# Kernel tuning notes

Measured on AMD Instinct MI355X. Metric: run time of the kernel, lower is better.

The kernel has to match this reference:

```python
import jax, jax.numpy as jnp
import numpy as np

ATTN_MASK_VALUE = -1e10
HEADS, DIM_HEAD, WSZ = 8, 64, 512


def ln(x, scale, eps=1e-5):
    # haiku LayerNorm(create_scale=True, create_offset=False, axis=-1)
    m = x.mean(-1, keepdims=True)
    v = ((x - m) ** 2).mean(-1, keepdims=True)
    return (x - m) / jnp.sqrt(v + eps) * scale


def local_attn(x, ln_s, qkv_w, ow, ob):
    n, _ = x.shape
    w = n // WSZ
    xn = ln(x, ln_s)
    qkv = xn @ qkv_w                                   # [n, 3*h*d]
    q, k, v = jnp.split(qkv, 3, axis=-1)
    resh = lambda t: t.reshape(w, WSZ, HEADS, DIM_HEAD).transpose(2, 0, 1, 3)  # h w n d
    q, k, v = resh(q), resh(k), resh(v)
    def lookback(t):
        t = jnp.pad(t, ((0, 0), (1, 0), (0, 0), (0, 0)))
        return jnp.concatenate((t[:, :-1], t[:, 1:]), axis=2)  # h w 2*wsz d
    k, v = lookback(k), lookback(v)
    sim = jnp.einsum('hwid,hwjd->hwij', q, k) * (DIM_HEAD ** -0.5)
    mask = jnp.tril(jnp.ones((WSZ, 2 * WSZ), dtype=bool), WSZ)
    sim = jnp.where(mask, sim, ATTN_MASK_VALUE)
    attn = jax.nn.softmax(sim, axis=-1)
    out = jnp.einsum('hwij,hwjd->hwid', attn, v)
    out = out.transpose(1, 2, 0, 3).reshape(n, HEADS * DIM_HEAD)
    return out @ ow + ob


def feedforward(x, ln_s, w1, b1, w2, b2):
    xn = ln(x, ln_s)
    return jax.nn.gelu(xn @ w1 + b1) @ w2 + b2


def gmlp(x, ln_s, win, bin_, sln, sw, sb, sow, sob, pow_, pob):
    n = x.shape[0]
    xn = ln(x, ln_s)
    h = jax.nn.gelu(xn @ win + bin_)                   # [n, d_ff]
    xg, gate = jnp.split(h, 2, axis=-1)                # [n, d_ff/2] each
    gate = ln(gate, sln)
    wm = sw * jnp.tril(jnp.ones((n, n), dtype=sw.dtype))
    gate = jnp.einsum('nd,mn->md', gate, wm) + sb      # causal spatial gate
    s = (xg * gate) @ sow + sob
    return s @ pow_ + pob


def forward(tokens, embed, attn_ln, attn_qkv, attn_ow, attn_ob,
            ff_ln, ff_w1, ff_b1, ff_w2, ff_b2,
            g_ln, g_win, g_bin, g_sln, g_sw, g_sb, g_sow, g_sob, g_pow, g_pob,
            fin_ln, head_w, head_b):
    x = embed[tokens]                                  # [n, dim]

    def block(xc, p):
        xc = xc + local_attn(xc, p['al'], p['aq'], p['aw'], p['ab'])
        xc = xc + feedforward(xc, p['fl'], p['f1'], p['fb1'], p['f2'], p['fb2'])
        return xc, None

    attn_params = {'al': attn_ln, 'aq': attn_qkv, 'aw': attn_ow, 'ab': attn_ob,
                   'fl': ff_ln, 'f1': ff_w1, 'fb1': ff_b1, 'f2': ff_w2, 'fb2': ff_b2}
    x, _ = jax.lax.scan(block, x, attn_params)

    def gblock(xc, p):
        xc = xc + gmlp(xc, p['l'], p['wi'], p['bi'], p['sl'], p['sw'], p['sb'],
                       p['so'], p['sob'], p['po'], p['pob'])
        return xc, None

    g_params = {'l': g_ln, 'wi': g_win, 'bi': g_bin, 'sl': g_sln, 'sw': g_sw,
                'sb': g_sb, 'so': g_sow, 'sob': g_sob, 'po': g_pow, 'pob': g_pob}
    x, _ = jax.lax.scan(gblock, x, g_params)

    return ln(x, fin_ln) @ head_w + head_b             # [n, num_tokens]


def setup_inputs() -> dict:
    key = jax.random.key(0)
    ks = jax.random.split(key, 16)
    n, dim, dff, inner, depth, gdepth, vocab = 2048, 1024, 4096, 512, 6, 2, 32
    sc = 0.02
    eps_sgu = 0.001 / n
    return {
        'tokens': jax.random.randint(ks[0], (n,), 0, vocab),
        'embed': jax.random.normal(ks[1], (vocab, dim)) * sc,
        'attn_ln': jnp.ones((depth, dim)),
        'attn_qkv': jax.random.normal(ks[2], (depth, dim, 3 * inner)) * sc,
        'attn_ow': jax.random.normal(ks[3], (depth, inner, dim)) * sc,
        'attn_ob': jnp.zeros((depth, dim)),
        'ff_ln': jnp.ones((depth, dim)),
        'ff_w1': jax.random.normal(ks[4], (depth, dim, dff)) * sc,
        'ff_b1': jnp.zeros((depth, dff)),
        'ff_w2': jax.random.normal(ks[5], (depth, dff, dim)) * sc,
        'ff_b2': jnp.zeros((depth, dim)),
        'g_ln': jnp.ones((gdepth, dim)),
        'g_win': jax.random.normal(ks[6], (gdepth, dim, dff)) * sc,
        'g_bin': jnp.zeros((gdepth, dff)),
        'g_sln': jnp.ones((gdepth, dff // 2)),
        'g_sw': jax.random.uniform(ks[7], (gdepth, n, n), minval=-eps_sgu, maxval=eps_sgu),
        'g_sb': jnp.ones((gdepth, n, 1)),
        'g_sow': jax.random.normal(ks[8], (gdepth, dff // 2, dff // 2)) * sc,
        'g_sob': jnp.zeros((gdepth, dff // 2)),
        'g_pow': jax.random.normal(ks[9], (gdepth, dff // 2, dim)) * sc,
        'g_pob': jnp.zeros((gdepth, dim)),
        'fin_ln': jnp.ones((dim,)),
        'head_w': jax.random.normal(ks[10], (dim, vocab)) * sc,
        'head_b': jnp.zeros((vocab,)),
    }


def reference(tokens, embed, attn_ln, attn_qkv, attn_ow, attn_ob,
              ff_ln, ff_w1, ff_b1, ff_w2, ff_b2,
              g_ln, g_win, g_bin, g_sln, g_sw, g_sb, g_sow, g_sob, g_pow, g_pob,
              fin_ln, head_w, head_b):
    return forward(tokens, embed, attn_ln, attn_qkv, attn_ow, attn_ob,
                   ff_ln, ff_w1, ff_b1, ff_w2, ff_b2,
                   g_ln, g_win, g_bin, g_sln, g_sw, g_sb, g_sow, g_sob, g_pow, g_pob,
                   fin_ln, head_w, head_b)
```

## Files before the change

### kernel.cpp

```cpp
#include <hip/hip_runtime.h>
#include <hip/hip_bf16.h>
#include <math.h>

using bf16 = __hip_bfloat16;
typedef __bf16 bf16x8 __attribute__((ext_vector_type(8)));
typedef float f32x4 __attribute__((ext_vector_type(4)));

__device__ __forceinline__ float toF(float v) { return v; }
__device__ __forceinline__ float toF(bf16 v) { return __bfloat162float(v); }

__device__ __forceinline__ float gelu_f(float x) {
  float t = tanhf(0.7978845608028654f * (x + 0.044715f * x * x * x));
  return 0.5f * x * (1.0f + t);
}

__device__ __forceinline__ void gld_lds16(const bf16* g, bf16* l) {
  __builtin_amdgcn_global_load_lds(
      (const __attribute__((address_space(1))) void*)g,
      (__attribute__((address_space(3))) void*)l, 16, 0, 0);
}

__device__ __forceinline__ float block_sum(float v) {
  __shared__ float tmp[8];
  int lane = threadIdx.x & 63, w = threadIdx.x >> 6, nw = blockDim.x >> 6;
#pragma unroll
  for (int o = 32; o > 0; o >>= 1) v += __shfl_down(v, o, 64);
  __syncthreads();
  if (lane == 0) tmp[w] = v;
  __syncthreads();
  float r = 0.f;
  for (int i = 0; i < nw; ++i) r += tmp[i];
  return r;
}

__device__ __forceinline__ float block_max(float v) {
  __shared__ float tmp2[8];
  int lane = threadIdx.x & 63, w = threadIdx.x >> 6, nw = blockDim.x >> 6;
#pragma unroll
  for (int o = 32; o > 0; o >>= 1) v = fmaxf(v, __shfl_down(v, o, 64));
  __syncthreads();
  if (lane == 0) tmp2[w] = v;
  __syncthreads();
  float r = -1e30f;
  for (int i = 0; i < nw; ++i) r = fmaxf(r, tmp2[i]);
  return r;
}

template <int BM, int BN, int EPI>
__launch_bounds__((BM / 64) * (BN / 64) * 64)
__global__ void gemm_bt(const bf16* __restrict__ A, int lda, long sAzh, long sAzw,
                        const bf16* __restrict__ B, int ldb, long sBzh, long sBzw,
                        void* __restrict__ C, int ldc, long sCzh, long sCzw,
                        int M, int N, int K, int zdiv,
                        const float* __restrict__ bias,
                        const float* __restrict__ rowbias,
                        const bf16* __restrict__ mul, int ldmul,
                        float* __restrict__ resid, int trilskip,
                        int nxk, int kchunk) {
  constexpr int BK = 32;
  constexpr int WM = BM / 64, WN = BN / 64;
  constexpr int NT = WM * WN * 64;
  __shared__ __align__(16) bf16 As[BM * BK];
  __shared__ __align__(16) bf16 Bs[BN * BK];
  const int tid = threadIdx.x;
  const int wave = tid >> 6, lane = tid & 63;
  const int wm = wave / WN, wn = wave % WN;
  int bx = blockIdx.x, kc = 0;
  if (kchunk > 0) { kc = bx / nxk; bx -= kc * nxk; }
  const int m0 = blockIdx.y * BM, n0 = bx * BN;
  const int z = blockIdx.z;
  const int zh = z / zdiv, zw = z % zdiv;
  A += zh * sAzh + zw * sAzw;
  B += zh * sBzh + zw * sBzw;
  const long coff = zh * sCzh + zw * sCzw;

  f32x4 acc[4][4];
#pragma unroll
  for (int i = 0; i < 4; ++i)
#pragma unroll
    for (int j = 0; j < 4; ++j)
#pragma unroll
      for (int r = 0; r < 4; ++r) acc[i][j][r] = 0.0f;

  const int kbeg = (kchunk > 0) ? kc * kchunk : 0;
  int kend = K;
  if (kchunk > 0 && kbeg + kchunk < kend) kend = kbeg + kchunk;
  if (trilskip && m0 + BM < kend) kend = m0 + BM;
  const int lrow = lane & 15, lk = (lane >> 4) << 3;

  for (int k0 = kbeg; k0 < kend; k0 += BK) {
#pragma unroll
    for (int c = 0; c < (BM * BK) / (NT * 8); ++c) {
      int e = (c * NT + tid) << 3;
      int r = e >> 5, kk = e & 31;
      gld_lds16(A + (long)(m0 + r) * lda + (k0 + kk), As + e);
    }
#pragma unroll
    for (int c = 0; c < (BN * BK) / (NT * 8); ++c) {
      int e = (c * NT + tid) << 3;
      int r = e >> 5, kk = e & 31;
      gld_lds16(B + (long)(n0 + r) * ldb + (k0 + kk), Bs + e);
    }
    __syncthreads();
    if (trilskip && (k0 + BK > m0)) {
#pragma unroll
      for (int c = 0; c < (BM * BK) / (NT * 8); ++c) {
        int e = (c * NT + tid) << 3;
        int r = e >> 5, kk = e & 31;
        int m = m0 + r;
#pragma unroll
        for (int q = 0; q < 8; ++q)
          if (k0 + kk + q > m) As[e + q] = __float2bfloat16(0.0f);
      }
      __syncthreads();
    }
    bf16x8 af[4], bg[4];
#pragma unroll
    for (int i = 0; i < 4; ++i)
      af[i] = *(const bf16x8*)(As + (wm * 64 + i * 16 + lrow) * BK + lk);
#pragma unroll
    for (int j = 0; j < 4; ++j)
      bg[j] = *(const bf16x8*)(Bs + (wn * 64 + j * 16 + lrow) * BK + lk);
#pragma unroll
    for (int i = 0; i < 4; ++i)
#pragma unroll
      for (int j = 0; j < 4; ++j)
        acc[i][j] = __builtin_amdgcn_mfma_f32_16x16x32_bf16(af[i], bg[j], acc[i][j], 0, 0, 0);
    __syncthreads();
  }

  const int rbase = m0 + wm * 64 + ((lane >> 4) << 2);
  const int cbase = n0 + wn * 64 + (lane & 15);
#pragma unroll
  for (int i = 0; i < 4; ++i) {
#pragma unroll
    for (int j = 0; j < 4; ++j) {
#pragma unroll
      for (int r = 0; r < 4; ++r) {
        int row = rbase + i * 16 + r;
        int col = cbase + j * 16;
        float v = acc[i][j][r];
        long idx = coff + (long)row * ldc + col;
        if (EPI == 0) {
          if (bias) v += bias[col];
          ((bf16*)C)[idx] = __float2bfloat16(v);
        } else if (EPI == 2) {
          v += bias[col];
          ((bf16*)C)[idx] = __float2bfloat16(gelu_f(v));
        } else if (EPI == 3) {
          if (kchunk > 0) {
            if (kbeg == 0) v += bias[col];
            atomicAdd(&resid[idx], v);
          } else {
            v += bias[col];
            resid[idx] += v;
          }
        } else if (EPI == 4) {
          v += rowbias[row];
          v *= __bfloat162float(mul[(long)row * ldmul + col]);
          ((bf16*)C)[idx] = __float2bfloat16(v);
        }
      }
    }
  }
}

__global__ void k_embed(const int* __restrict__ tokens, const float* __restrict__ embed,
                        float* __restrict__ x) {
  int t = blockIdx.x;
  int tok = tokens[t];
  for (int j = threadIdx.x; j < 1024; j += 256)
    x[(long)t * 1024 + j] = embed[(long)tok * 1024 + j];
}

template <typename TIN>
__global__ void k_ln(const TIN* __restrict__ in, int ldin, const float* __restrict__ scale,
                     bf16* __restrict__ out, int ldout, int C) {
  int row = blockIdx.x, tid = threadIdx.x;
  const TIN* p = in + (long)row * ldin;
  float loc[8];
  int nper = C >> 8;
  float s = 0.f;
  for (int c = 0; c < nper; ++c) {
    float v = toF(p[c * 256 + tid]);
    loc[c] = v;
    s += v;
  }
  s = block_sum(s);
  float mean = s / (float)C;
  float s2 = 0.f;
  for (int c = 0; c < nper; ++c) {
    float d = loc[c] - mean;
    s2 += d * d;
  }
  s2 = block_sum(s2);
  float inv = 1.0f / sqrtf(s2 / (float)C + 1e-5f);
  for (int c = 0; c < nper; ++c) {
    int j = c * 256 + tid;
    out[(long)row * ldout + j] = __float2bfloat16((loc[c] - mean) * inv * scale[j]);
  }
}

template <typename TIN>
__global__ void k_transpose(const TIN* __restrict__ in, int ldin, bf16* __restrict__ out,
                            int ldout, int rows, int cols) {
  __shared__ bf16 tile[32][33];
  int c0 = blockIdx.x * 32, r0 = blockIdx.y * 32;
  int tx = threadIdx.x & 31, ty = threadIdx.x >> 5;
#pragma unroll
  for (int j = 0; j < 32; j += 8)
    tile[ty + j][tx] = __float2bfloat16(toF(in[(long)(r0 + ty + j) * ldin + c0 + tx]));
  __syncthreads();
#pragma unroll
  for (int j = 0; j < 32; j += 8)
    out[(long)(c0 + ty + j) * ldout + r0 + tx] = tile[tx][ty + j];
}

__global__ void k_cast(const float* __restrict__ in, bf16* __restrict__ out, long n) {
  long i = (long)blockIdx.x * 256 + threadIdx.x;
  if (i < n) out[i] = __float2bfloat16(in[i]);
}

__global__ void k_packk(const bf16* __restrict__ qkv, bf16* __restrict__ kpad) {
  int idx = blockIdx.x * 256 + threadIdx.x;
  int d = idx & 63, t = (idx >> 6) & 2047, h = idx >> 17;
  kpad[(long)h * 163840 + (512 + t) * 64 + d] = qkv[(long)t * 1536 + 512 + h * 64 + d];
}

__global__ void k_zeropad(bf16* __restrict__ kpad, bf16* __restrict__ vtpad) {
  int idx = blockIdx.x * 256 + threadIdx.x;
  bf16 z = __float2bfloat16(0.0f);
  if (idx < 262144) {
    int h = idx >> 15, off = idx & 32767;
    kpad[(long)h * 163840 + off] = z;
  } else {
    int i = idx - 262144;
    int f = i >> 9, j = i & 511;
    vtpad[(long)f * 2560 + j] = z;
  }
}

__global__ void k_softmax(bf16* __restrict__ SP) {
  int row = blockIdx.x;
  int i = row & 511;
  int limit = i + 513;
  bf16* s = SP + (long)row * 1024;
  int tid = threadIdx.x;
  float v[4];
  float mx = -1e30f;
#pragma unroll
  for (int c = 0; c < 4; ++c) {
    int j = c * 256 + tid;
    float xv = (j < limit) ? __bfloat162float(s[j]) * 0.125f : -1e30f;
    v[c] = xv;
    mx = fmaxf(mx, xv);
  }
  mx = block_max(mx);
  float sum = 0.f;
#pragma unroll
  for (int c = 0; c < 4; ++c) {
    float e = (v[c] <= -1e29f) ? 0.f : expf(v[c] - mx);
    v[c] = e;
    sum += e;
  }
  sum = block_sum(sum);
  float inv = 1.0f / sum;
#pragma unroll
  for (int c = 0; c < 4; ++c) {
    int j = c * 256 + tid;
    s[j] = __float2bfloat16(v[c] * inv);
  }
}

__global__ void k_head(const float* __restrict__ x, const float* __restrict__ sc,
                       const float* __restrict__ w, const float* __restrict__ b,
                       float* __restrict__ out) {
  int row = blockIdx.x, tid = threadIdx.x;
  __shared__ float xn[1024];
  const float* p = x + (long)row * 1024;
  float loc[4];
  float s = 0.f;
#pragma unroll
  for (int c = 0; c < 4; ++c) {
    float v = p[c * 256 + tid];
    loc[c] = v;
    s += v;
  }
  s = block_sum(s);
  float mean = s / 1024.f;
  float s2 = 0.f;
#pragma unroll
  for (int c = 0; c < 4; ++c) {
    float d = loc[c] - mean;
    s2 += d * d;
  }
  s2 = block_sum(s2);
  float inv = 1.0f / sqrtf(s2 / 1024.f + 1e-5f);
#pragma unroll
  for (int c = 0; c < 4; ++c) {
    int j = c * 256 + tid;
    xn[j] = (loc[c] - mean) * inv * sc[j];
  }
  __syncthreads();
  int t = tid & 31, sl = tid >> 5;
  float partial = 0.f;
  for (int kk = 0; kk < 128; ++kk) {
    int k = sl * 128 + kk;
    partial += xn[k] * w[k * 32 + t];
  }
  __shared__ float red[256];
  red[tid] = partial;
  __syncthreads();
  if (tid < 32) {
    float r = 0.f;
    for (int q = 0; q < 8; ++q) r += red[q * 32 + t];
    out[(long)row * 32 + t] = r + b[t];
  }
}

extern "C" void kernel_launch(void* const* d_in, const int* in_sizes, int n_in,
                              void* d_out, int out_size, void* d_ws, size_t ws_size,
                              hipStream_t stream) {
  (void)in_sizes; (void)n_in; (void)out_size; (void)ws_size;
  const int*   tokens   = (const int*)d_in[0];
  const float* embed    = (const float*)d_in[1];
  const float* attn_ln  = (const float*)d_in[2];
  const float* attn_qkv = (const float*)d_in[3];
  const float* attn_ow  = (const float*)d_in[4];
  const float* attn_ob  = (const float*)d_in[5];
  const float* ff_ln    = (const float*)d_in[6];
  const float* ff_w1    = (const float*)d_in[7];
  const float* ff_b1    = (const float*)d_in[8];
  const float* ff_w2    = (const float*)d_in[9];
  const float* ff_b2    = (const float*)d_in[10];
  const float* g_ln     = (const float*)d_in[11];
  const float* g_win    = (const float*)d_in[12];
  const float* g_bin    = (const float*)d_in[13];
  const float* g_sln    = (const float*)d_in[14];
  const float* g_sw     = (const float*)d_in[15];
  const float* g_sb     = (const float*)d_in[16];
  const float* g_sow    = (const float*)d_in[17];
  const float* g_sob    = (const float*)d_in[18];
  const float* g_pow    = (const float*)d_in[19];
  const float* g_pob    = (const float*)d_in[20];
  const float* fin_ln   = (const float*)d_in[21];
  const float* head_w   = (const float*)d_in[22];
  const float* head_b   = (const float*)d_in[23];

  char* ws = (char*)d_ws;
  float* x  = (float*)ws;
  bf16* xn  = (bf16*)(ws + 8388608);
  char* SC  = ws + 12582912;
  bf16* qkv   = (bf16*)SC;
  bf16* kpad  = (bf16*)(SC + 6291456);
  bf16* vtpad = (bf16*)(SC + 8912896);
  bf16* SP    = (bf16*)(SC + 11534336);
  bf16* att   = (bf16*)(SC + 45088768);
  bf16* h      = (bf16*)SC;
  bf16* gateLN = (bf16*)(SC + 16777216);
  bf16* gateT  = (bf16*)(SC + 25165824);
  bf16* prod   = (bf16*)(SC + 33554432);
  bf16* sbuf   = (bf16*)(SC + 41943040);
  bf16* W  = (bf16*)(ws + 62914560);
  bf16* W2 = (bf16*)(ws + 71303168);

  k_embed<<<2048, 256, 0, stream>>>(tokens, embed, x);

  for (int L = 0; L < 6; ++L) {
    const float* qkvw = attn_qkv + (long)L * 1024 * 1536;
    const float* oww  = attn_ow + (long)L * 512 * 1024;
    const float* w1   = ff_w1 + (long)L * 1024 * 4096;
    const float* w2   = ff_w2 + (long)L * 4096 * 1024;

    k_ln<float><<<2048, 256, 0, stream>>>(x, 1024, attn_ln + L * 1024, xn, 1024, 1024);
    k_transpose<float><<<dim3(48, 32), 256, 0, stream>>>(qkvw, 1536, W, 1024, 1024, 1536);
    gemm_bt<128, 128, 0><<<dim3(12, 16, 1), 256, 0, stream>>>(
        xn, 1024, 0, 0, W, 1024, 0, 0, qkv, 1536, 0, 0,
        2048, 1536, 1024, 1, nullptr, nullptr, nullptr, 0, nullptr, 0, 0, 0);

    k_packk<<<4096, 256, 0, stream>>>(qkv, kpad);
    k_zeropad<<<2048, 256, 0, stream>>>(kpad, vtpad);
    k_transpose<bf16><<<dim3(16, 64), 256, 0, stream>>>(qkv + 1024, 1536, vtpad + 512, 2560, 2048, 512);

    gemm_bt<128, 128, 0><<<dim3(8, 4, 32), 256, 0, stream>>>(
        qkv, 1536, 64, 786432, kpad, 64, 163840, 32768, SP, 1024, 2097152, 524288,
        512, 1024, 64, 4, nullptr, nullptr, nullptr, 0, nullptr, 0, 0, 0);
    k_softmax<<<16384, 256, 0, stream>>>(SP);
    gemm_bt<128, 64, 0><<<dim3(1, 4, 32), 128, 0, stream>>>(
        SP, 1024, 2097152, 524288, vtpad, 2560, 163840, 512, att, 512, 64, 262144,
        512, 64, 1024, 4, nullptr, nullptr, nullptr, 0, nullptr, 0, 0, 0);
    k_transpose<float><<<dim3(32, 16), 256, 0, stream>>>(oww, 1024, W, 512, 512, 1024);
    gemm_bt<128, 128, 3><<<dim3(16, 16, 1), 256, 0, stream>>>(
        att, 512, 0, 0, W, 512, 0, 0, nullptr, 1024, 0, 0,
        2048, 1024, 512, 1, attn_ob + L * 1024, nullptr, nullptr, 0, x, 0, 8, 256);

    k_ln<float><<<2048, 256, 0, stream>>>(x, 1024, ff_ln + L * 1024, xn, 1024, 1024);
    k_transpose<float><<<dim3(128, 32), 256, 0, stream>>>(w1, 4096, W, 1024, 1024, 4096);
    gemm_bt<128, 128, 2><<<dim3(32, 16, 1), 256, 0, stream>>>(
        xn, 1024, 0, 0, W, 1024, 0, 0, h, 4096, 0, 0,
        2048, 4096, 1024, 1, ff_b1 + L * 4096, nullptr, nullptr, 0, nullptr, 0, 0, 0);
    k_transpose<float><<<dim3(32, 128), 256, 0, stream>>>(w2, 1024, W, 4096, 4096, 1024);
    gemm_bt<128, 128, 3><<<dim3(32, 16, 1), 256, 0, stream>>>(
        h, 4096, 0, 0, W, 4096, 0, 0, nullptr, 1024, 0, 0,
        2048, 1024, 4096, 1, ff_b2 + L * 1024, nullptr, nullptr, 0, x, 0, 8, 1024);
  }

  for (int G = 0; G < 2; ++G) {
    const float* winw = g_win + (long)G * 1024 * 4096;
    const float* soww = g_sow + (long)G * 2048 * 2048;
    const float* poww = g_pow + (long)G * 2048 * 1024;

    k_ln<float><<<2048, 256, 0, stream>>>(x, 1024, g_ln + G * 1024, xn, 1024, 1024);
    k_transpose<float><<<dim3(128, 32), 256, 0, stream>>>(winw, 4096, W, 1024, 1024, 4096);
    gemm_bt<128, 128, 2><<<dim3(32, 16, 1), 256, 0, stream>>>(
        xn, 1024, 0, 0, W, 1024, 0, 0, h, 4096, 0, 0,
        2048, 4096, 1024, 1, g_bin + G * 4096, nullptr, nullptr, 0, nullptr, 0, 0, 0);
    k_ln<bf16><<<2048, 256, 0, stream>>>(h + 2048, 4096, g_sln + G * 2048, gateLN, 2048, 2048);
    k_transpose<bf16><<<dim3(64, 64), 256, 0, stream>>>(gateLN, 2048, gateT, 2048, 2048, 2048);
    k_cast<<<16384, 256, 0, stream>>>(g_sw + (long)G * 2048 * 2048, W2, 4194304L);
    gemm_bt<128, 128, 4><<<dim3(16, 16, 1), 256, 0, stream>>>(
        W2, 2048, 0, 0, gateT, 2048, 0, 0, prod, 2048, 0, 0,
        2048, 2048, 2048, 1, nullptr, g_sb + G * 2048, h, 4096, nullptr, 1, 0, 0);
    k_transpose<float><<<dim3(64, 64), 256, 0, stream>>>(soww, 2048, W, 2048, 2048, 2048);
    gemm_bt<128, 128, 0><<<dim3(16, 16, 1), 256, 0, stream>>>(
        prod, 2048, 0, 0, W, 2048, 0, 0, sbuf, 2048, 0, 0,
        2048, 2048, 2048, 1, g_sob + G * 2048, nullptr, nullptr, 0, nullptr, 0, 0, 0);
    k_transpose<float><<<dim3(32, 64), 256, 0, stream>>>(poww, 1024, W, 2048, 2048, 1024);
    gemm_bt<128, 128, 3><<<dim3(32, 16, 1), 256, 0, stream>>>(
        sbuf, 2048, 0, 0, W, 2048, 0, 0, nullptr, 1024, 0, 0,
        2048, 1024, 2048, 1, g_pob + G * 1024, nullptr, nullptr, 0, x, 0, 8, 512);
  }

  k_head<<<2048, 256, 0, stream>>>(x, fin_ln, head_w, head_b, (float*)d_out);
}
```

Before: 2.350 ms.

## Double-buffer GEMM LDS tiles with BK=64 and split-K the attention PV product

The GEMM kernel gains template parameters for K-tile depth (now 64) and double-buffering, so the next tile's global-to-LDS load is issued while the current tile is computed. Most GEMMs switch to the double-buffered BK=64 variant. The attn·V GEMM, which previously launched only 128 blocks, is split four ways along K with fp32 atomic accumulation into a zeroed buffer and a cast back to bf16. This raises parallelism at the cost of extra zero/cast kernels and atomics. The double-buffered path has no barrier between issuing async global_load_lds and reading the buffer, so it may race.

```diff
diff --git a/kernel.cpp b/kernel.cpp
--- a/kernel.cpp
+++ b/kernel.cpp
@@ -46,7 +46,7 @@
   return r;
 }
 
-template <int BM, int BN, int EPI>
+template <int BM, int BN, int EPI, int BK, int DBUF>
 __launch_bounds__((BM / 64) * (BN / 64) * 64)
 __global__ void gemm_bt(const bf16* __restrict__ A, int lda, long sAzh, long sAzw,
                         const bf16* __restrict__ B, int ldb, long sBzh, long sBzw,
@@ -57,11 +57,13 @@
                         const bf16* __restrict__ mul, int ldmul,
                         float* __restrict__ resid, int trilskip,
                         int nxk, int kchunk) {
-  constexpr int BK = 32;
+  constexpr int LBK = (BK == 64) ? 6 : 5;
   constexpr int WM = BM / 64, WN = BN / 64;
   constexpr int NT = WM * WN * 64;
-  __shared__ __align__(16) bf16 As[BM * BK];
-  __shared__ __align__(16) bf16 Bs[BN * BK];
+  constexpr int ACH = (BM * BK) / (NT * 8);
+  constexpr int BCH = (BN * BK) / (NT * 8);
+  __shared__ __align__(16) bf16 As[(DBUF ? 2 : 1) * BM * BK];
+  __shared__ __align__(16) bf16 Bs[(DBUF ? 2 : 1) * BN * BK];
   const int tid = threadIdx.x;
   const int wave = tid >> 6, lane = tid & 63;
   const int wm = wave / WN, wn = wave % WN;
@@ -88,45 +90,73 @@
   if (trilskip && m0 + BM < kend) kend = m0 + BM;
   const int lrow = lane & 15, lk = (lane >> 4) << 3;
 
-  for (int k0 = kbeg; k0 < kend; k0 += BK) {
-#pragma unroll
-    for (int c = 0; c < (BM * BK) / (NT * 8); ++c) {
+  auto stage = [&](int sel, int k0) {
+    bf16* Ad = As + sel * BM * BK;
+    bf16* Bd = Bs + sel * BN * BK;
+#pragma unroll
+    for (int c = 0; c < ACH; ++c) {
       int e = (c * NT + tid) << 3;
-      int r = e >> 5, kk = e & 31;
-      gld_lds16(A + (long)(m0 + r) * lda + (k0 + kk), As + e);
-    }
-#pragma unroll
-    for (int c = 0; c < (BN * BK) / (NT * 8); ++c) {
+      int r = e >> LBK, kk = e & (BK - 1);
+      gld_lds16(A + (long)(m0 + r) * lda + (k0 + kk), Ad + e);
+    }
+#pragma unroll
+    for (int c = 0; c < BCH; ++c) {
       int e = (c * NT + tid) << 3;
-      int r = e >> 5, kk = e & 31;
-      gld_lds16(B + (long)(n0 + r) * ldb + (k0 + kk), Bs + e);
-    }
+      int r = e >> LBK, kk = e & (BK - 1);
+      gld_lds16(B + (long)(n0 + r) * ldb + (k0 + kk), Bd + e);
+    }
+  };
+  auto zero_diag = [&](int sel, int k0) {
+    bf16* Ad = As + sel * BM * BK;
+#pragma unroll
+    for (int c = 0; c < ACH; ++c) {
+      int e = (c * NT + tid) << 3;
+      int r = e >> LBK, kk = e & (BK - 1);
+      int m = m0 + r;
+#pragma unroll
+      for (int q = 0; q < 8; ++q)
+        if (k0 + kk + q > m) Ad[e + q] = __float2bfloat16(0.0f);
+    }
+  };
+  auto compute = [&](int sel) {
+    const bf16* Ad = As + sel * BM * BK;
+    const bf16* Bd = Bs + sel * BN * BK;
+#pragma unroll
+    for (int kk2 = 0; kk2 < BK; kk2 += 32) {
+      bf16x8 af[4], bg[4];
+#pragma unroll
+      for (int i = 0; i < 4; ++i)
+        af[i] = *(const bf16x8*)(Ad + (wm * 64 + i * 16 + lrow) * BK + kk2 + lk);
+#pragma unroll
+      for (int j = 0; j < 4; ++j)
+        bg[j] = *(const bf16x8*)(Bd + (wn * 64 + j * 16 + lrow) * BK + kk2 + lk);
+#pragma unroll
+      for (int i = 0; i < 4; ++i)
+#pragma unroll
+        for (int j = 0; j < 4; ++j)
+          acc[i][j] = __builtin_amdgcn_mfma_f32_16x16x32_bf16(af[i], bg[j], acc[i][j], 0, 0, 0);
+    }
+  };
+
+  if constexpr (DBUF) {
+    int cur = 0;
+    stage(0, kbeg);
     __syncthreads();
-    if (trilskip && (k0 + BK > m0)) {
-#pragma unroll
-      for (int c = 0; c < (BM * BK) / (NT * 8); ++c) {
-        int e = (c * NT + tid) << 3;
-        int r = e >> 5, kk = e & 31;
-        int m = m0 + r;
-#pragma unroll
-        for (int q = 0; q < 8; ++q)
-          if (k0 + kk + q > m) As[e + q] = __float2bfloat16(0.0f);
-      }
+    for (int k0 = kbeg; k0 < kend; k0 += BK) {
+      if (k0 + BK < kend) stage(cur ^ 1, k0 + BK);
+      if (trilskip && (k0 + BK > m0)) { zero_diag(cur, k0); __syncthreads(); }
+      compute(cur);
       __syncthreads();
-    }
-    bf16x8 af[4], bg[4];
-#pragma unroll
-    for (int i = 0; i < 4; ++i)
-      af[i] = *(const bf16x8*)(As + (wm * 64 + i * 16 + lrow) * BK + lk);
-#pragma unroll
-    for (int j = 0; j < 4; ++j)
-      bg[j] = *(const bf16x8*)(Bs + (wn * 64 + j * 16 + lrow) * BK + lk);
-#pragma unroll
-    for (int i = 0; i < 4; ++i)
-#pragma unroll
-      for (int j = 0; j < 4; ++j)
-        acc[i][j] = __builtin_amdgcn_mfma_f32_16x16x32_bf16(af[i], bg[j], acc[i][j], 0, 0, 0);
-    __syncthreads();
+      cur ^= 1;
+    }
+  } else {
+    for (int k0 = kbeg; k0 < kend; k0 += BK) {
+      stage(0, k0);
+      __syncthreads();
+      if (trilskip && (k0 + BK > m0)) { zero_diag(0, k0); __syncthreads(); }
+      compute(0);
+      __syncthreads();
+    }
   }
 
   const int rbase = m0 + wm * 64 + ((lane >> 4) << 2);
@@ -149,10 +179,10 @@
           ((bf16*)C)[idx] = __float2bfloat16(gelu_f(v));
         } else if (EPI == 3) {
           if (kchunk > 0) {
-            if (kbeg == 0) v += bias[col];
+            if (kbeg == 0 && bias) v += bias[col];
             atomicAdd(&resid[idx], v);
           } else {
-            v += bias[col];
+            if (bias) v += bias[col];
             resid[idx] += v;
           }
         } else if (EPI == 4) {
@@ -219,6 +249,11 @@
 __global__ void k_cast(const float* __restrict__ in, bf16* __restrict__ out, long n) {
   long i = (long)blockIdx.x * 256 + threadIdx.x;
   if (i < n) out[i] = __float2bfloat16(in[i]);
+}
+
+__global__ void k_zerof(float* __restrict__ p, long n) {
+  long i = (long)blockIdx.x * 256 + threadIdx.x;
+  if (i < n) p[i] = 0.0f;
 }
 
 __global__ void k_packk(const bf16* __restrict__ qkv, bf16* __restrict__ kpad) {
@@ -363,6 +398,7 @@
   bf16* sbuf   = (bf16*)(SC + 41943040);
   bf16* W  = (bf16*)(ws + 62914560);
   bf16* W2 = (bf16*)(ws + 71303168);
+  float* att_f32 = (float*)(ws + 71303168);
 
   k_embed<<<2048, 256, 0, stream>>>(tokens, embed, x);
 
@@ -374,7 +410,7 @@
 
     k_ln<float><<<2048, 256, 0, stream>>>(x, 1024, attn_ln + L * 1024, xn, 1024, 1024);
     k_transpose<float><<<dim3(48, 32), 256, 0, stream>>>(qkvw, 1536, W, 1024, 1024, 1536);
-    gemm_bt<128, 128, 0><<<dim3(12, 16, 1), 256, 0, stream>>>(
+    gemm_bt<128, 128, 0, 64, 1><<<dim3(12, 16, 1), 256, 0, stream>>>(
         xn, 1024, 0, 0, W, 1024, 0, 0, qkv, 1536, 0, 0,
         2048, 1536, 1024, 1, nullptr, nullptr, nullptr, 0, nullptr, 0, 0, 0);
 
@@ -382,25 +418,27 @@
     k_zeropad<<<2048, 256, 0, stream>>>(kpad, vtpad);
     k_transpose<bf16><<<dim3(16, 64), 256, 0, stream>>>(qkv + 1024, 1536, vtpad + 512, 2560, 2048, 512);
 
-    gemm_bt<128, 128, 0><<<dim3(8, 4, 32), 256, 0, stream>>>(
+    gemm_bt<128, 128, 0, 64, 0><<<dim3(8, 4, 32), 256, 0, stream>>>(
         qkv, 1536, 64, 786432, kpad, 64, 163840, 32768, SP, 1024, 2097152, 524288,
         512, 1024, 64, 4, nullptr, nullptr, nullptr, 0, nullptr, 0, 0, 0);
     k_softmax<<<16384, 256, 0, stream>>>(SP);
-    gemm_bt<128, 64, 0><<<dim3(1, 4, 32), 128, 0, stream>>>(
-        SP, 1024, 2097152, 524288, vtpad, 2560, 163840, 512, att, 512, 64, 262144,
-        512, 64, 1024, 4, nullptr, nullptr, nullptr, 0, nullptr, 0, 0, 0);
+    k_zerof<<<4096, 256, 0, stream>>>(att_f32, 1048576L);
+    gemm_bt<128, 64, 3, 64, 1><<<dim3(4, 4, 32), 128, 0, stream>>>(
+        SP, 1024, 2097152, 524288, vtpad, 2560, 163840, 512, nullptr, 512, 64, 262144,
+        512, 64, 1024, 4, nullptr, nullptr, nullptr, 0, att_f32, 0, 1, 256);
+    k_cast<<<4096, 256, 0, stream>>>(att_f32, att, 1048576L);
     k_transpose<float><<<dim3(32, 16), 256, 0, stream>>>(oww, 1024, W, 512, 512, 1024);
-    gemm_bt<128, 128, 3><<<dim3(16, 16, 1), 256, 0, stream>>>(
+    gemm_bt<128, 128, 3, 64, 1><<<dim3(16, 16, 1), 256, 0, stream>>>(
         att, 512, 0, 0, W, 512, 0, 0, nullptr, 1024, 0, 0,
         2048, 1024, 512, 1, attn_ob + L * 1024, nullptr, nullptr, 0, x, 0, 8, 256);
 
     k_ln<float><<<2048, 256, 0, stream>>>(x, 1024, ff_ln + L * 1024, xn, 1024, 1024);
     k_transpose<float><<<dim3(128, 32), 256, 0, stream>>>(w1, 4096, W, 1024, 1024, 4096);
-    gemm_bt<128, 128, 2><<<dim3(32, 16, 1), 256, 0, stream>>>(
+    gemm_bt<128, 128, 2, 64, 1><<<dim3(32, 16, 1), 256, 0, stream>>>(
         xn, 1024, 0, 0, W, 1024, 0, 0, h, 4096, 0, 0,
         2048, 4096, 1024, 1, ff_b1 + L * 4096, nullptr, nullptr, 0, nullptr, 0, 0, 0);
     k_transpose<float><<<dim3(32, 128), 256, 0, stream>>>(w2, 1024, W, 4096, 4096, 1024);
-    gemm_bt<128, 128, 3><<<dim3(32, 16, 1), 256, 0, stream>>>(
+    gemm_bt<128, 128, 3, 64, 1><<<dim3(32, 16, 1), 256, 0, stream>>>(
         h, 4096, 0, 0, W, 4096, 0, 0, nullptr, 1024, 0, 0,
         2048, 1024, 4096, 1, ff_b2 + L * 1024, nullptr, nullptr, 0, x, 0, 8, 1024);
   }
@@ -412,21 +450,21 @@
 
     k_ln<float><<<2048, 256, 0, stream>>>(x, 1024, g_ln + G * 1024, xn, 1024, 1024);
     k_transpose<float><<<dim3(128, 32), 256, 0, stream>>>(winw, 4096, W, 1024, 1024, 4096);
-    gemm_bt<128, 128, 2><<<dim3(32, 16, 1), 256, 0, stream>>>(
+    gemm_bt<128, 128, 2, 64, 1><<<dim3(32, 16, 1), 256, 0, stream>>>(
         xn, 1024, 0, 0, W, 1024, 0, 0, h, 4096, 0, 0,
         2048, 4096, 1024, 1, g_bin + G * 4096, nullptr, nullptr, 0, nullptr, 0, 0, 0);
     k_ln<bf16><<<2048, 256, 0, stream>>>(h + 2048, 4096, g_sln + G * 2048, gateLN, 2048, 2048);
     k_transpose<bf16><<<dim3(64, 64), 256, 0, stream>>>(gateLN, 2048, gateT, 2048, 2048, 2048);
     k_cast<<<16384, 256, 0, stream>>>(g_sw + (long)G * 2048 * 2048, W2, 4194304L);
-    gemm_bt<128, 128, 4><<<dim3(16, 16, 1), 256, 0, stream>>>(
+    gemm_bt<128, 128, 4, 64, 1><<<dim3(16, 16, 1), 256, 0, stream>>>(
         W2, 2048, 0, 0, gateT, 2048, 0, 0, prod, 2048, 0, 0,
         2048, 2048, 2048, 1, nullptr, g_sb + G * 2048, h, 4096, nullptr, 1, 0, 0);
     k_transpose<float><<<dim3(64, 64), 256, 0, stream>>>(soww, 2048, W, 2048, 2048, 2048);
-    gemm_bt<128, 128, 0><<<dim3(16, 16, 1), 256, 0, stream>>>(
+    gemm_bt<128, 128, 0, 64, 1><<<dim3(16, 16, 1), 256, 0, stream>>>(
         prod, 2048, 0, 0, W, 2048, 0, 0, sbuf, 2048, 0, 0,
         2048, 2048, 2048, 1, g_sob + G * 2048, nullptr, nullptr, 0, nullptr, 0, 0, 0);
     k_transpose<float><<<dim3(32, 64), 256, 0, stream>>>(poww, 1024, W, 2048, 2048, 1024);
-    gemm_bt<128, 128, 3><<<dim3(32, 16, 1), 256, 0, stream>>>(
+    gemm_bt<128, 128, 3, 64, 1><<<dim3(32, 16, 1), 256, 0, stream>>>(
         sbuf, 2048, 0, 0, W, 2048, 0, 0, nullptr, 1024, 0, 0,
         2048, 1024, 2048, 1, g_pob + G * 1024, nullptr, nullptr, 0, x, 0, 8, 512);
   }
```

After: 2.404 ms. 1.02x slower.
